# Kernel optimization log

Measured on AMD Instinct MI355X. Metric: run time of the kernel, lower is better.

The kernel has to match this reference:

```python
import jax, jax.numpy as jnp
import numpy as np

P_EPS = 1e-6            # nn.PairwiseDistance default eps
ALPHA = 0.25
STD_TARGET = 1.0
NUM_COMMUNITIES = 512   # C = number of unique community ids
BIG = 1e30              # masking value for hard-negative min


def setup_inputs() -> dict:
    key = jax.random.key(0)
    k1, k2, k3 = jax.random.split(key, 3)
    B, N, D, C = 1, 100000, 128, NUM_COMMUNITIES
    node_features = jax.random.normal(k1, (B, N, D), dtype=jnp.float32)
    # row 0: a permutation of node indices; row 1: community of that node.
    perm = jax.random.permutation(k2, N).astype(jnp.int32)
    comm_per_node = jnp.concatenate([
        jnp.arange(C, dtype=jnp.int32),  # guarantee every community appears
        jax.random.randint(k3, (N - C,), 0, C, dtype=jnp.int32),
    ])
    community_belong_list = jnp.stack([perm, comm_per_node[perm]])  # [2, N]
    return {"node_features": node_features, "community_belong_list": community_belong_list}


def reference(node_features, community_belong_list):
    B, N, D = node_features.shape
    C = NUM_COMMUNITIES
    dt = node_features.dtype

    # ---- _community_inverse_permute: invert row-0 permutation, reorder columns ----
    perm = community_belong_list[0]
    inv = jnp.zeros((N,), perm.dtype).at[perm].add(jnp.arange(N, dtype=perm.dtype))
    cbl = community_belong_list[:, inv]          # row0 == arange(N) after this
    comm = cbl[1]                                # [N] community id per node
    src = node_features[:, cbl[0], :]            # [B,N,D] gather (identity order)

    # ---- groupby sum / count -> community means ----
    comm_sum = jnp.zeros((B, C, D), dt).at[:, comm, :].add(src)        # [B,C,D]
    counts = jnp.zeros((C,), dt).at[comm].add(jnp.asarray(1.0, dt))   # [C]
    comm_mean = comm_sum / counts[None, :, None]                      # [B,C,D]

    # ---- cdist(node_features, comm_mean, p=2) -> [B,N,C] ----
    x2 = jnp.sum(node_features * node_features, -1)                   # [B,N]
    c2 = jnp.sum(comm_mean * comm_mean, -1)                           # [B,C]
    dots = jnp.einsum('bnd,bcd->bnc', node_features, comm_mean)
    distance = jnp.sqrt(jnp.maximum(x2[:, :, None] + c2[:, None, :] - 2.0 * dots, 0.0))

    # ---- leave-one-out community mean per node, positive distance ----
    cnt_pn = counts[comm]                                             # [N]
    cnt_m1 = jnp.maximum(cnt_pn - 1.0, 1.0)                           # [N]
    x_minus = jnp.where((cnt_pn == 1.0)[None, :, None], jnp.asarray(0.0, dt), src)
    loo_mean = (comm_sum[:, comm, :] - x_minus) / cnt_m1[None, :, None]
    pos_dist = jnp.sqrt(jnp.sum((loo_mean - src + P_EPS) ** 2, -1))   # [B,N]

    # ---- negatives: all communities except the node's own ----
    own = distance[:, jnp.arange(N), comm]                            # [B,N]
    mean_neg = (jnp.sum(distance, -1) - own) / (C - 1)                # [B,N]
    pos_mask = jnp.zeros((N, C), bool).at[jnp.arange(N), comm].set(True)
    hard_neg = jnp.min(jnp.where(pos_mask[None], jnp.asarray(BIG, dt), distance), -1)

    trip_mean = jnp.maximum(pos_dist - mean_neg + ALPHA, 0.0)
    trip_min = jnp.maximum(pos_dist - hard_neg + ALPHA, 0.0)

    # ---- groupby std (unbiased) per community per feature ----
    sq = jnp.zeros((B, C, D), dt).at[:, comm, :].add((src - comm_mean[:, comm, :]) ** 2)
    std = jnp.sqrt(sq / jnp.maximum(counts - 1.0, 1.0)[None, :, None])

    return (trip_mean.mean(), trip_min.mean(), ((std - STD_TARGET) ** 2).mean())
```

## Files before the change

### kernel.cpp

```cpp
#include <hip/hip_runtime.h>

#define NCOMM 512
#define DIM   128
#define ALPHA 0.25f
#define PEPS  1e-6f
#define BIGF  1e30f
#define TILE_C 16
#define NT    (NCOMM / TILE_C)

typedef __attribute__((ext_vector_type(8))) _Float16 f16x8;
typedef __attribute__((ext_vector_type(4))) float f32x4;

#define GLOAD_LDS16(g, l) __builtin_amdgcn_global_load_lds( \
    (const __attribute__((address_space(1))) void*)(g), \
    (__attribute__((address_space(3))) void*)(l), 16, 0, 0)


__global__ void k_inv(const int* __restrict__ cbl, int* __restrict__ inv, int N) {
    int i = blockIdx.x * 256 + threadIdx.x;
    if (i < N) inv[cbl[i]] = i;
}

__global__ void k_comm(const int* __restrict__ cbl, const int* __restrict__ inv,
                       int* __restrict__ comm, int* __restrict__ idx0,
                       int* __restrict__ counts, int N) {
    __shared__ int h[NCOMM];
    int t = threadIdx.x;
    h[t] = 0; h[t + 256] = 0;
    __syncthreads();
    int j = blockIdx.x * 256 + t;
    if (j < N) {
        int ij = inv[j];
        int c  = cbl[N + ij];
        comm[j] = c;
        idx0[j] = cbl[ij];
        atomicAdd(&h[c], 1);
    }
    __syncthreads();
    int v = h[t];        if (v) atomicAdd(&counts[t], v);
    v = h[t + 256];      if (v) atomicAdd(&counts[t + 256], v);
}

__global__ void k_scan(const int* __restrict__ counts, int* __restrict__ offsets,
                       int* __restrict__ cursor, float* __restrict__ countf) {
    __shared__ int sc[NCOMM];
    int t = threadIdx.x;
    int v0 = counts[t];
    sc[t] = v0;
    __syncthreads();
    for (int off = 1; off < NCOMM; off <<= 1) {
        int v = (t >= off) ? sc[t - off] : 0;
        __syncthreads();
        sc[t] += v;
        __syncthreads();
    }
    int excl = sc[t] - v0;
    offsets[t] = excl;
    cursor[t]  = excl;
    countf[t]  = (float)v0;
}

__global__ void k_sort(const int* __restrict__ comm, int* __restrict__ cursor,
                       int* __restrict__ sorted, int N) {
    __shared__ int h[NCOMM], hb[NCOMM];
    int t = threadIdx.x;
    h[t] = 0; h[t + 256] = 0;
    __syncthreads();
    int j0 = blockIdx.x * 1024 + t;
    int cs[4];
    #pragma unroll
    for (int q = 0; q < 4; ++q) {
        int j = j0 + q * 256;
        cs[q] = (j < N) ? comm[j] : -1;
        if (cs[q] >= 0) atomicAdd(&h[cs[q]], 1);
    }
    __syncthreads();
    int v = h[t];        if (v) hb[t] = atomicAdd(&cursor[t], v);
    v = h[t + 256];      if (v) hb[t + 256] = atomicAdd(&cursor[t + 256], v);
    __syncthreads();
    #pragma unroll
    for (int q = 0; q < 4; ++q) {
        int j = j0 + q * 256;
        if (cs[q] >= 0) {
            int p = atomicAdd(&hb[cs[q]], 1);
            sorted[p] = j;
        }
    }
}


__global__ void __launch_bounds__(256) k_stats(
        const float* __restrict__ NF, const int* __restrict__ idx0,
        const int* __restrict__ sorted, const int* __restrict__ offsets,
        const int* __restrict__ counts,
        float* __restrict__ comm_sum,
        _Float16* __restrict__ CMh, _Float16* __restrict__ CMl,
        float* __restrict__ c2, float* __restrict__ accum) {
    __shared__ int ridx[512];
    __shared__ float4 bufS[256], bufQ[256];
    int c = blockIdx.x, t = threadIdx.x;
    int d4 = t & 31, r = t >> 5;
    int cnt = counts[c], base = offsets[c];
    const float4* NF4 = (const float4*)NF;

    float4 s4 = make_float4(0.f, 0.f, 0.f, 0.f);
    float4 q4 = make_float4(0.f, 0.f, 0.f, 0.f);
    for (int chunk = 0; chunk < cnt; chunk += 512) {
        int m = min(cnt - chunk, 512);
        for (int i = t; i < m; i += 256) ridx[i] = idx0[sorted[base + chunk + i]];
        __syncthreads();
        for (int i = r; i < m; i += 8) {
            float4 v = NF4[(size_t)ridx[i] * 32 + d4];
            s4.x += v.x; s4.y += v.y; s4.z += v.z; s4.w += v.w;
            q4.x = fmaf(v.x, v.x, q4.x); q4.y = fmaf(v.y, v.y, q4.y);
            q4.z = fmaf(v.z, v.z, q4.z); q4.w = fmaf(v.w, v.w, q4.w);
        }
        __syncthreads();
    }
    bufS[t] = s4; bufQ[t] = q4;
    __syncthreads();
    if (t < 128) {
        float4 a = bufS[t], b = bufS[t + 128];
        a.x += b.x; a.y += b.y; a.z += b.z; a.w += b.w; bufS[t] = a;
        float4 e = bufQ[t], f = bufQ[t + 128];
        e.x += f.x; e.y += f.y; e.z += f.z; e.w += f.w; bufQ[t] = e;
    }
    __syncthreads();
    if (t < 64) {
        float4 a = bufS[t], b = bufS[t + 64];
        a.x += b.x; a.y += b.y; a.z += b.z; a.w += b.w; bufS[t] = a;
        float4 e = bufQ[t], f = bufQ[t + 64];
        e.x += f.x; e.y += f.y; e.z += f.z; e.w += f.w; bufQ[t] = e;
    }
    __syncthreads();
    if (t < 32) {
        float4 a = bufS[t], b = bufS[t + 32];
        a.x += b.x; a.y += b.y; a.z += b.z; a.w += b.w;
        float4 e = bufQ[t], f = bufQ[t + 32];
        e.x += f.x; e.y += f.y; e.z += f.z; e.w += f.w;
        float sarr[4] = {a.x, a.y, a.z, a.w};
        float qarr[4] = {e.x, e.y, e.z, e.w};
        float cf = (float)cnt;
        float mm = 0.f, ee = 0.f;
        #pragma unroll
        for (int k = 0; k < 4; ++k) {
            int d = t * 4 + k;
            float s = sarr[k];
            comm_sum[c * DIM + d] = s;
            float m = (cnt > 0) ? s / cf : 0.f;
            _Float16 mh = (_Float16)m;
            CMh[c * DIM + d] = mh;
            CMl[c * DIM + d] = (_Float16)(m - (float)mh);
            float varn = fmaxf(fmaf(-cf * m, m, qarr[k]), 0.f);
            float stdv = sqrtf(varn / fmaxf(cf - 1.f, 1.f));
            float er = stdv - 1.f;
            mm = fmaf(m, m, mm);
            ee = fmaf(er, er, ee);
        }
        #pragma unroll
        for (int msk = 1; msk < 32; msk <<= 1) {
            mm += __shfl_xor(mm, msk);
            ee += __shfl_xor(ee, msk);
        }
        if (t == 0) {
            c2[c] = mm;
            atomicAdd(&accum[2], ee);
        }
    }
}


__global__ void __launch_bounds__(256, 2) k_main(
        const float* __restrict__ NF,
        const _Float16* __restrict__ CMh,
        const _Float16* __restrict__ CMl,
        const float* __restrict__ comm_sum,
        const float* __restrict__ c2g,
        const float* __restrict__ countf,
        const int* __restrict__ comm,
        const int* __restrict__ idx0,
        float* __restrict__ accum, int N) {
    __shared__ _Float16 Bst[4][2][2][TILE_C * DIM];
    __shared__ float c2s[NCOMM];
    __shared__ int   comms[256];
    __shared__ float x2s[256];
    __shared__ float sums[256], mins[256];
    __shared__ float red[8];

    int tid = threadIdx.x;
    int w  = tid >> 6;
    int l  = tid & 63;
    int lr = l & 15;
    int lk = l >> 4;
    int n0 = blockIdx.x * 256;

    int goff[4];
    #pragma unroll
    for (int i = 0; i < 4; ++i) {
        int p = i * 64 + l;
        int row = p >> 4, cp = p & 15;
        goff[i] = (row * 16 + (cp ^ row)) * 8;
    }
    auto stage = [&](int tt, int b) {
        int base = tt * (TILE_C * DIM);
        _Float16* lh = &Bst[w][b][0][0];
        _Float16* ll = &Bst[w][b][1][0];
        #pragma unroll
        for (int i = 0; i < 4; ++i) {
            GLOAD_LDS16(CMh + base + goff[i], lh + i * 512);
            GLOAD_LDS16(CMl + base + goff[i], ll + i * 512);
        }
    };
    stage(0, 0);

    c2s[tid]       = c2g[tid];
    c2s[tid + 256] = c2g[tid + 256];
    {
        int gn = n0 + tid;
        comms[tid] = (gn < N) ? comm[gn] : -1;
    }

    f16x8 ah[4][4];
    #pragma unroll
    for (int mf = 0; mf < 4; ++mf) {
        int n = n0 + w * 64 + mf * 16 + lr;
        const float4* src = (const float4*)NF + (size_t)n * 32 + lk * 2;
        float p2 = 0.f;
        #pragma unroll
        for (int ks = 0; ks < 4; ++ks) {
            float4 v0 = make_float4(0.f, 0.f, 0.f, 0.f), v1 = v0;
            if (n < N) { v0 = src[ks * 8]; v1 = src[ks * 8 + 1]; }
            float fr[8] = {v0.x, v0.y, v0.z, v0.w, v1.x, v1.y, v1.z, v1.w};
            f16x8 hh;
            #pragma unroll
            for (int t = 0; t < 8; ++t) {
                hh[t] = (_Float16)fr[t];
                p2 = fmaf(fr[t], fr[t], p2);
            }
            ah[mf][ks] = hh;
        }
        p2 += __shfl_xor(p2, 16);
        p2 += __shfl_xor(p2, 32);
        if (lk == 0) x2s[w * 64 + mf * 16 + lr] = -0.5f * p2;
    }
    __syncthreads();

    int cnv[4][4];
    float sumv[4][4], minv[4][4];
    #pragma unroll
    for (int mf = 0; mf < 4; ++mf)
        #pragma unroll
        for (int j = 0; j < 4; ++j) {
            cnv[mf][j] = comms[w * 64 + mf * 16 + lk * 4 + j];
            sumv[mf][j] = 0.f; minv[mf][j] = BIGF;
        }

    int buf = 0;
    for (int tt = 0; tt < NT; ++tt) {
        if (tt + 1 < NT) {
            stage(tt + 1, buf ^ 1);
            asm volatile("s_waitcnt vmcnt(8)" ::: "memory");
        } else {
            asm volatile("s_waitcnt vmcnt(0)" ::: "memory");
        }
        __builtin_amdgcn_sched_barrier(0);

        const _Float16* bhp = &Bst[w][buf][0][0];
        const _Float16* blp = &Bst[w][buf][1][0];
        f16x8 bh[4], bl[4];
        #pragma unroll
        for (int ks = 0; ks < 4; ++ks) {
            int ch = (ks * 4 + lk) ^ lr;
            bh[ks] = *(const f16x8*)&bhp[(size_t)(lr * 16 + ch) * 8];
            bl[ks] = *(const f16x8*)&blp[(size_t)(lr * 16 + ch) * 8];
        }
        f32x4 acc[4];
        #pragma unroll
        for (int mf = 0; mf < 4; ++mf)
            acc[mf] = *(const f32x4*)&x2s[w * 64 + mf * 16 + lk * 4];

        #pragma unroll
        for (int ks = 0; ks < 4; ++ks) {
            #pragma unroll
            for (int mf = 0; mf < 4; ++mf)
                acc[mf] = __builtin_amdgcn_mfma_f32_16x16x32_f16(ah[mf][ks], bh[ks], acc[mf], 0, 0, 0);
            #pragma unroll
            for (int mf = 0; mf < 4; ++mf)
                acc[mf] = __builtin_amdgcn_mfma_f32_16x16x32_f16(ah[mf][ks], bl[ks], acc[mf], 0, 0, 0);
        }

        int ccol = tt * TILE_C + lr;
        float c2v = c2s[ccol];
        #pragma unroll
        for (int mf = 0; mf < 4; ++mf)
            #pragma unroll
            for (int j = 0; j < 4; ++j) {
                float d2 = fmaf(-2.f, acc[mf][j], c2v);
                float da = __builtin_amdgcn_sqrtf(fmaxf(d2, 0.f));
                sumv[mf][j] += da;
                minv[mf][j] = fminf(minv[mf][j], (cnv[mf][j] == ccol) ? BIGF : da);
            }
        buf ^= 1;
    }

    #pragma unroll
    for (int mf = 0; mf < 4; ++mf)
        #pragma unroll
        for (int j = 0; j < 4; ++j) {
            float sv = sumv[mf][j], mv = minv[mf][j];
            #pragma unroll
            for (int msk = 1; msk < 16; msk <<= 1) {
                sv += __shfl_xor(sv, msk);
                mv = fminf(mv, __shfl_xor(mv, msk));
            }
            if (lr == 0) {
                int idx = w * 64 + mf * 16 + lk * 4 + j;
                sums[idx] = sv; mins[idx] = mv;
            }
        }
    __syncthreads();

    float tmean = 0.f, tminv = 0.f;
    {
        int ln = tid;
        int n = n0 + ln;
        if (n < N) {
            int cnode = comms[ln];
            float cf  = countf[cnode];
            float cm1 = fmaxf(cf - 1.f, 1.f);
            float rs  = 1.f / cm1;
            bool single = (cf == 1.f);
            const float4* srow = (const float4*)(NF + (size_t)idx0[n] * DIM);
            const float4* csum = (const float4*)(comm_sum + (size_t)cnode * DIM);
            float q = 0.f, dot = 0.f;
            #pragma unroll 8
            for (int m = 0; m < 32; ++m) {
                float4 sv = srow[m];
                float4 cs = csum[m];
                float4 xm = single ? make_float4(0.f, 0.f, 0.f, 0.f) : sv;
                float lx = (cs.x - xm.x) * rs - sv.x + PEPS;
                float ly = (cs.y - xm.y) * rs - sv.y + PEPS;
                float lz = (cs.z - xm.z) * rs - sv.z + PEPS;
                float lw = (cs.w - xm.w) * rs - sv.w + PEPS;
                q = fmaf(lx, lx, fmaf(ly, ly, fmaf(lz, lz, fmaf(lw, lw, q))));
                dot = fmaf(sv.x, cs.x, fmaf(sv.y, cs.y, fmaf(sv.z, cs.z, fmaf(sv.w, cs.w, dot))));
            }
            float pos = sqrtf(q);
            float x2 = -2.f * x2s[ln];
            float ownd2 = x2 + c2s[cnode] - 2.f * (dot / cf);
            float own = sqrtf(fmaxf(ownd2, 0.f));
            float mean_neg = (sums[ln] - own) * (1.f / (float)(NCOMM - 1));
            tmean = fmaxf(pos - mean_neg + ALPHA, 0.f);
            tminv = fmaxf(pos - mins[ln] + ALPHA, 0.f);
        }
    }
    #pragma unroll
    for (int msk = 1; msk < 64; msk <<= 1) {
        tmean += __shfl_xor(tmean, msk);
        tminv += __shfl_xor(tminv, msk);
    }
    if ((tid & 63) == 0) { red[w * 2] = tmean; red[w * 2 + 1] = tminv; }
    __syncthreads();
    if (tid == 0) {
        atomicAdd(&accum[0], red[0] + red[2] + red[4] + red[6]);
        atomicAdd(&accum[1], red[1] + red[3] + red[5] + red[7]);
    }
}

__global__ void k_final(const float* __restrict__ accum, float* __restrict__ out, int N) {
    if (threadIdx.x == 0) {
        out[0] = accum[0] / (float)N;
        out[1] = accum[1] / (float)N;
        out[2] = accum[2] / (float)(NCOMM * DIM);
    }
}


extern "C" void kernel_launch(void* const* d_in, const int* in_sizes, int n_in,
                              void* d_out, int out_size, void* d_ws, size_t ws_size,
                              hipStream_t stream) {
    const float* NF  = (const float*)d_in[0];
    const int*   CBL = (const int*)d_in[1];
    int N = in_sizes[1] / 2;
    if (N <= 0) return;

    char* ws = (char*)d_ws;
    float* accum   = (float*)ws;
    int*   counts  = (int*)(ws + 16);
    int*   cursor  = (int*)(ws + 16 + 2048);
    int*   offsets = (int*)(ws + 16 + 2 * 2048);
    float* countf  = (float*)(ws + 16 + 3 * 2048);
    float* c2      = (float*)(ws + 16 + 4 * 2048);
    char* p = ws + 16 + 5 * 2048;
    int* inv    = (int*)p; p += (size_t)N * 4;
    int* comm   = (int*)p; p += (size_t)N * 4;
    int* idx0   = (int*)p; p += (size_t)N * 4;
    int* sorted = (int*)p; p += (size_t)N * 4;
    float* comm_sum = (float*)p; p += (size_t)NCOMM * DIM * 4;
    _Float16* CMh = (_Float16*)p; p += (size_t)NCOMM * DIM * 2;
    _Float16* CMl = (_Float16*)p;

    hipMemsetAsync(d_ws, 0, 16 + 2048, stream);

    int nb = (N + 255) / 256;
    k_inv <<<nb, 256, 0, stream>>>(CBL, inv, N);
    k_comm<<<nb, 256, 0, stream>>>(CBL, inv, comm, idx0, counts, N);
    k_scan<<<1, NCOMM, 0, stream>>>(counts, offsets, cursor, countf);
    int nb4 = (N + 1023) / 1024;
    k_sort<<<nb4, 256, 0, stream>>>(comm, cursor, sorted, N);
    k_stats<<<NCOMM, 256, 0, stream>>>(NF, idx0, sorted, offsets, counts,
                                       comm_sum, CMh, CMl, c2, accum);
    int mb = (N + 255) / 256;
    k_main<<<mb, 256, 0, stream>>>(NF, CMh, CMl, comm_sum, c2, countf,
                                   comm, idx0, accum, N);
    k_final<<<1, 64, 0, stream>>>(accum, (float*)d_out, N);
}
```

Baseline: 129.9 us.

## Load centroid fragments directly into registers and halve rows per block

The main distance kernel drops the LDS staging of fp16 centroid tiles. Each wave now loads its B fragments straight from global memory into registers, using two register buffers alternated by hand. Each block covers 128 rows instead of 256, the occupancy hint is raised to 3, and the per-node positive-distance tail is split across two threads joined with a shuffle. The idx0 gather array is removed because composing the permutation with its inverse gives the identity, which saves a write and several indirect reads. The trade-off is that doubling the block count doubles total centroid reads through the cache.

Result: slower. 197.9 us (+52.4%).

```diff
diff --git a/kernel.cpp b/kernel.cpp
--- a/kernel.cpp
+++ b/kernel.cpp
@@ -11,10 +11,6 @@
 typedef __attribute__((ext_vector_type(8))) _Float16 f16x8;
 typedef __attribute__((ext_vector_type(4))) float f32x4;
 
-#define GLOAD_LDS16(g, l) __builtin_amdgcn_global_load_lds( \
-    (const __attribute__((address_space(1))) void*)(g), \
-    (__attribute__((address_space(3))) void*)(l), 16, 0, 0)
-
 
 __global__ void k_inv(const int* __restrict__ cbl, int* __restrict__ inv, int N) {
     int i = blockIdx.x * 256 + threadIdx.x;
@@ -22,18 +18,15 @@
 }
 
 __global__ void k_comm(const int* __restrict__ cbl, const int* __restrict__ inv,
-                       int* __restrict__ comm, int* __restrict__ idx0,
-                       int* __restrict__ counts, int N) {
+                       int* __restrict__ comm, int* __restrict__ counts, int N) {
     __shared__ int h[NCOMM];
     int t = threadIdx.x;
     h[t] = 0; h[t + 256] = 0;
     __syncthreads();
     int j = blockIdx.x * 256 + t;
     if (j < N) {
-        int ij = inv[j];
-        int c  = cbl[N + ij];
+        int c = cbl[N + inv[j]];
         comm[j] = c;
-        idx0[j] = cbl[ij];
         atomicAdd(&h[c], 1);
     }
     __syncthreads();
@@ -90,7 +83,7 @@
 
 
 __global__ void __launch_bounds__(256) k_stats(
-        const float* __restrict__ NF, const int* __restrict__ idx0,
+        const float* __restrict__ NF,
         const int* __restrict__ sorted, const int* __restrict__ offsets,
         const int* __restrict__ counts,
         float* __restrict__ comm_sum,
@@ -107,7 +100,7 @@
     float4 q4 = make_float4(0.f, 0.f, 0.f, 0.f);
     for (int chunk = 0; chunk < cnt; chunk += 512) {
         int m = min(cnt - chunk, 512);
-        for (int i = t; i < m; i += 256) ridx[i] = idx0[sorted[base + chunk + i]];
+        for (int i = t; i < m; i += 256) ridx[i] = sorted[base + chunk + i];
         __syncthreads();
         for (int i = r; i < m; i += 8) {
             float4 v = NF4[(size_t)ridx[i] * 32 + d4];
@@ -170,7 +163,7 @@
 }
 
 
-__global__ void __launch_bounds__(256, 2) k_main(
+__global__ void __launch_bounds__(256, 3) k_main(
         const float* __restrict__ NF,
         const _Float16* __restrict__ CMh,
         const _Float16* __restrict__ CMl,
@@ -178,13 +171,11 @@
         const float* __restrict__ c2g,
         const float* __restrict__ countf,
         const int* __restrict__ comm,
-        const int* __restrict__ idx0,
         float* __restrict__ accum, int N) {
-    __shared__ _Float16 Bst[4][2][2][TILE_C * DIM];
     __shared__ float c2s[NCOMM];
-    __shared__ int   comms[256];
-    __shared__ float x2s[256];
-    __shared__ float sums[256], mins[256];
+    __shared__ int   comms[128];
+    __shared__ float x2sh[128];
+    __shared__ float sums[128], mins[128];
     __shared__ float red[8];
 
     int tid = threadIdx.x;
@@ -192,38 +183,19 @@
     int l  = tid & 63;
     int lr = l & 15;
     int lk = l >> 4;
-    int n0 = blockIdx.x * 256;
-
-    int goff[4];
-    #pragma unroll
-    for (int i = 0; i < 4; ++i) {
-        int p = i * 64 + l;
-        int row = p >> 4, cp = p & 15;
-        goff[i] = (row * 16 + (cp ^ row)) * 8;
-    }
-    auto stage = [&](int tt, int b) {
-        int base = tt * (TILE_C * DIM);
-        _Float16* lh = &Bst[w][b][0][0];
-        _Float16* ll = &Bst[w][b][1][0];
-        #pragma unroll
-        for (int i = 0; i < 4; ++i) {
-            GLOAD_LDS16(CMh + base + goff[i], lh + i * 512);
-            GLOAD_LDS16(CMl + base + goff[i], ll + i * 512);
-        }
-    };
-    stage(0, 0);
+    int n0 = blockIdx.x * 128;
 
     c2s[tid]       = c2g[tid];
     c2s[tid + 256] = c2g[tid + 256];
-    {
+    if (tid < 128) {
         int gn = n0 + tid;
         comms[tid] = (gn < N) ? comm[gn] : -1;
     }
 
-    f16x8 ah[4][4];
-    #pragma unroll
-    for (int mf = 0; mf < 4; ++mf) {
-        int n = n0 + w * 64 + mf * 16 + lr;
+    f16x8 ah[2][4];
+    #pragma unroll
+    for (int mf = 0; mf < 2; ++mf) {
+        int n = n0 + w * 32 + mf * 16 + lr;
         const float4* src = (const float4*)NF + (size_t)n * 32 + lk * 2;
         float p2 = 0.f;
         #pragma unroll
@@ -241,70 +213,70 @@
         }
         p2 += __shfl_xor(p2, 16);
         p2 += __shfl_xor(p2, 32);
-        if (lk == 0) x2s[w * 64 + mf * 16 + lr] = -0.5f * p2;
-    }
-    __syncthreads();
-
-    int cnv[4][4];
-    float sumv[4][4], minv[4][4];
-    #pragma unroll
-    for (int mf = 0; mf < 4; ++mf)
+        if (lk == 0) x2sh[w * 32 + mf * 16 + lr] = -0.5f * p2;
+    }
+    __syncthreads();
+
+    f32x4 x2v[2];
+    int cnv[2][4];
+    float sumv[2][4], minv[2][4];
+    #pragma unroll
+    for (int mf = 0; mf < 2; ++mf) {
+        x2v[mf] = *(const f32x4*)&x2sh[w * 32 + mf * 16 + lk * 4];
         #pragma unroll
         for (int j = 0; j < 4; ++j) {
-            cnv[mf][j] = comms[w * 64 + mf * 16 + lk * 4 + j];
+            cnv[mf][j] = comms[w * 32 + mf * 16 + lk * 4 + j];
             sumv[mf][j] = 0.f; minv[mf][j] = BIGF;
         }
-
-    int buf = 0;
-    for (int tt = 0; tt < NT; ++tt) {
-        if (tt + 1 < NT) {
-            stage(tt + 1, buf ^ 1);
-            asm volatile("s_waitcnt vmcnt(8)" ::: "memory");
-        } else {
-            asm volatile("s_waitcnt vmcnt(0)" ::: "memory");
-        }
-        __builtin_amdgcn_sched_barrier(0);
-
-        const _Float16* bhp = &Bst[w][buf][0][0];
-        const _Float16* blp = &Bst[w][buf][1][0];
-        f16x8 bh[4], bl[4];
+    }
+
+    const f16x8* BH = (const f16x8*)CMh + (lr * 16 + lk);
+    const f16x8* BL = (const f16x8*)CMl + (lr * 16 + lk);
+
+    auto loadB = [&](f16x8* bh, f16x8* bl, int tt) {
+        const f16x8* ph = BH + tt * 256;
+        const f16x8* pl = BL + tt * 256;
         #pragma unroll
         for (int ks = 0; ks < 4; ++ks) {
-            int ch = (ks * 4 + lk) ^ lr;
-            bh[ks] = *(const f16x8*)&bhp[(size_t)(lr * 16 + ch) * 8];
-            bl[ks] = *(const f16x8*)&blp[(size_t)(lr * 16 + ch) * 8];
-        }
-        f32x4 acc[4];
-        #pragma unroll
-        for (int mf = 0; mf < 4; ++mf)
-            acc[mf] = *(const f32x4*)&x2s[w * 64 + mf * 16 + lk * 4];
-
+            bh[ks] = ph[ks * 4];
+            bl[ks] = pl[ks * 4];
+        }
+    };
+    auto compute = [&](const f16x8* bh, const f16x8* bl, int tt) {
+        f32x4 acc0 = x2v[0], acc1 = x2v[1];
         #pragma unroll
         for (int ks = 0; ks < 4; ++ks) {
-            #pragma unroll
-            for (int mf = 0; mf < 4; ++mf)
-                acc[mf] = __builtin_amdgcn_mfma_f32_16x16x32_f16(ah[mf][ks], bh[ks], acc[mf], 0, 0, 0);
-            #pragma unroll
-            for (int mf = 0; mf < 4; ++mf)
-                acc[mf] = __builtin_amdgcn_mfma_f32_16x16x32_f16(ah[mf][ks], bl[ks], acc[mf], 0, 0, 0);
-        }
-
+            acc0 = __builtin_amdgcn_mfma_f32_16x16x32_f16(ah[0][ks], bh[ks], acc0, 0, 0, 0);
+            acc1 = __builtin_amdgcn_mfma_f32_16x16x32_f16(ah[1][ks], bh[ks], acc1, 0, 0, 0);
+            acc0 = __builtin_amdgcn_mfma_f32_16x16x32_f16(ah[0][ks], bl[ks], acc0, 0, 0, 0);
+            acc1 = __builtin_amdgcn_mfma_f32_16x16x32_f16(ah[1][ks], bl[ks], acc1, 0, 0, 0);
+        }
         int ccol = tt * TILE_C + lr;
         float c2v = c2s[ccol];
         #pragma unroll
-        for (int mf = 0; mf < 4; ++mf)
-            #pragma unroll
-            for (int j = 0; j < 4; ++j) {
-                float d2 = fmaf(-2.f, acc[mf][j], c2v);
-                float da = __builtin_amdgcn_sqrtf(fmaxf(d2, 0.f));
-                sumv[mf][j] += da;
-                minv[mf][j] = fminf(minv[mf][j], (cnv[mf][j] == ccol) ? BIGF : da);
-            }
-        buf ^= 1;
-    }
-
-    #pragma unroll
-    for (int mf = 0; mf < 4; ++mf)
+        for (int j = 0; j < 4; ++j) {
+            float d2a = fmaf(-2.f, acc0[j], c2v);
+            float da  = __builtin_amdgcn_sqrtf(fmaxf(d2a, 0.f));
+            sumv[0][j] += da;
+            minv[0][j] = fminf(minv[0][j], (cnv[0][j] == ccol) ? BIGF : da);
+            float d2b = fmaf(-2.f, acc1[j], c2v);
+            float db  = __builtin_amdgcn_sqrtf(fmaxf(d2b, 0.f));
+            sumv[1][j] += db;
+            minv[1][j] = fminf(minv[1][j], (cnv[1][j] == ccol) ? BIGF : db);
+        }
+    };
+
+    f16x8 bhA[4], blA[4], bhB[4], blB[4];
+    loadB(bhA, blA, 0);
+    for (int tt = 0; tt < NT; tt += 2) {
+        loadB(bhB, blB, tt + 1);
+        compute(bhA, blA, tt);
+        loadB(bhA, blA, (tt + 2 < NT) ? tt + 2 : NT - 1);
+        compute(bhB, blB, tt + 1);
+    }
+
+    #pragma unroll
+    for (int mf = 0; mf < 2; ++mf)
         #pragma unroll
         for (int j = 0; j < 4; ++j) {
             float sv = sumv[mf][j], mv = minv[mf][j];
@@ -314,7 +286,7 @@
                 mv = fminf(mv, __shfl_xor(mv, msk));
             }
             if (lr == 0) {
-                int idx = w * 64 + mf * 16 + lk * 4 + j;
+                int idx = w * 32 + mf * 16 + lk * 4 + j;
                 sums[idx] = sv; mins[idx] = mv;
             }
         }
@@ -322,7 +294,7 @@
 
     float tmean = 0.f, tminv = 0.f;
     {
-        int ln = tid;
+        int ln = tid >> 1, half = tid & 1;
         int n = n0 + ln;
         if (n < N) {
             int cnode = comms[ln];
@@ -330,11 +302,11 @@
             float cm1 = fmaxf(cf - 1.f, 1.f);
             float rs  = 1.f / cm1;
             bool single = (cf == 1.f);
-            const float4* srow = (const float4*)(NF + (size_t)idx0[n] * DIM);
-            const float4* csum = (const float4*)(comm_sum + (size_t)cnode * DIM);
+            const float4* srow = (const float4*)NF + (size_t)n * 32 + half * 16;
+            const float4* csum = (const float4*)(comm_sum + (size_t)cnode * DIM) + half * 16;
             float q = 0.f, dot = 0.f;
-            #pragma unroll 8
-            for (int m = 0; m < 32; ++m) {
+            #pragma unroll
+            for (int m = 0; m < 16; ++m) {
                 float4 sv = srow[m];
                 float4 cs = csum[m];
                 float4 xm = single ? make_float4(0.f, 0.f, 0.f, 0.f) : sv;
@@ -345,13 +317,17 @@
                 q = fmaf(lx, lx, fmaf(ly, ly, fmaf(lz, lz, fmaf(lw, lw, q))));
                 dot = fmaf(sv.x, cs.x, fmaf(sv.y, cs.y, fmaf(sv.z, cs.z, fmaf(sv.w, cs.w, dot))));
             }
-            float pos = sqrtf(q);
-            float x2 = -2.f * x2s[ln];
-            float ownd2 = x2 + c2s[cnode] - 2.f * (dot / cf);
-            float own = sqrtf(fmaxf(ownd2, 0.f));
-            float mean_neg = (sums[ln] - own) * (1.f / (float)(NCOMM - 1));
-            tmean = fmaxf(pos - mean_neg + ALPHA, 0.f);
-            tminv = fmaxf(pos - mins[ln] + ALPHA, 0.f);
+            q   += __shfl_xor(q, 1);
+            dot += __shfl_xor(dot, 1);
+            if (half == 0) {
+                float pos = sqrtf(q);
+                float x2 = -2.f * x2sh[ln];
+                float ownd2 = x2 + c2s[cnode] - 2.f * (dot / cf);
+                float own = sqrtf(fmaxf(ownd2, 0.f));
+                float mean_neg = (sums[ln] - own) * (1.f / (float)(NCOMM - 1));
+                tmean = fmaxf(pos - mean_neg + ALPHA, 0.f);
+                tminv = fmaxf(pos - mins[ln] + ALPHA, 0.f);
+            }
         }
     }
     #pragma unroll
@@ -394,7 +370,6 @@
     char* p = ws + 16 + 5 * 2048;
     int* inv    = (int*)p; p += (size_t)N * 4;
     int* comm   = (int*)p; p += (size_t)N * 4;
-    int* idx0   = (int*)p; p += (size_t)N * 4;
     int* sorted = (int*)p; p += (size_t)N * 4;
     float* comm_sum = (float*)p; p += (size_t)NCOMM * DIM * 4;
     _Float16* CMh = (_Float16*)p; p += (size_t)NCOMM * DIM * 2;
@@ -404,14 +379,14 @@
 
     int nb = (N + 255) / 256;
     k_inv <<<nb, 256, 0, stream>>>(CBL, inv, N);
-    k_comm<<<nb, 256, 0, stream>>>(CBL, inv, comm, idx0, counts, N);
+    k_comm<<<nb, 256, 0, stream>>>(CBL, inv, comm, counts, N);
     k_scan<<<1, NCOMM, 0, stream>>>(counts, offsets, cursor, countf);
     int nb4 = (N + 1023) / 1024;
     k_sort<<<nb4, 256, 0, stream>>>(comm, cursor, sorted, N);
-    k_stats<<<NCOMM, 256, 0, stream>>>(NF, idx0, sorted, offsets, counts,
+    k_stats<<<NCOMM, 256, 0, stream>>>(NF, sorted, offsets, counts,
                                        comm_sum, CMh, CMl, c2, accum);
-    int mb = (N + 255) / 256;
+    int mb = (N + 127) / 128;
     k_main<<<mb, 256, 0, stream>>>(NF, CMh, CMl, comm_sum, c2, countf,
-                                   comm, idx0, accum, N);
+                                   comm, accum, N);
     k_final<<<1, 64, 0, stream>>>(accum, (float*)d_out, N);
 }
```
